# Optimization experiments

Hardware: AMD Instinct MI355X
Metric: run time of the kernel (lower is better)

Reference implementation:

```python
import jax, jax.numpy as jnp
import numpy as np

N, DIN, DOUT = 8192, 64, 32
EPS_F = 1e-6


def setup_inputs() -> dict:
    key = jax.random.key(0)
    k_x, k_q, k_lam, k_f, k_b = jax.random.split(key, 5)
    x = jax.random.normal(k_x, (N, DIN), dtype=jnp.float32)
    # Q_S stands in for the eigenvector matrix of the normalized adjacency;
    # scale by 1/sqrt(N) so columns have ~unit norm like an orthonormal basis.
    Q_S = jax.random.normal(k_q, (N, N), dtype=jnp.float32) / np.float32(np.sqrt(N))
    # Eigenvalues of D^-1/2 (A+I) D^-1/2 lie in [-1, 1].
    Lambda_S = jax.random.uniform(k_lam, (N,), dtype=jnp.float32, minval=-1.0, maxval=1.0)
    # Xavier-uniform init for F (din x din): bound = sqrt(6/(din+din))
    bound_f = np.float32(np.sqrt(6.0 / (DIN + DIN)))
    F = jax.random.uniform(k_f, (DIN, DIN), dtype=jnp.float32, minval=-bound_f, maxval=bound_f)
    # nn.Linear default init for B: U(-1/sqrt(din), 1/sqrt(din))
    bound_b = np.float32(1.0 / np.sqrt(DIN))
    B_w = jax.random.uniform(k_b, (DOUT, DIN), dtype=jnp.float32, minval=-bound_b, maxval=bound_b)
    gamma = jnp.float32(0.8)
    return {"x": x, "Q_S": Q_S, "Lambda_S": Lambda_S, "F": F, "B_w": B_w, "gamma": gamma}


def reference(x, Q_S, Lambda_S, F, B_w, gamma):
    # g(F) = F^T F / (||F^T F||_F + eps): symmetric PSD with Frobenius norm <= 1
    FF = F.T @ F
    gF = FF / (jnp.linalg.norm(FF) + EPS_F)
    lam_F, Q_F = jnp.linalg.eigh(gF)                      # [d], [d, d]
    # G[i, j] = 1 / (1 - gamma * lam_F[i] * lam_S[j])      # [d, N]
    G = 1.0 / (1.0 - gamma * lam_F[:, None] * Lambda_S[None, :])
    Xt = x.T                                              # [d, N]
    # Z = Q_F (G * (Q_F^T X^T Q_S)) Q_S^T  -- spectral-domain equilibrium solve
    Z = Q_F @ (G * (Q_F.T @ Xt @ Q_S)) @ Q_S.T            # [d, N]
    return Z.T @ B_w.T                                    # [N, dout]
```

## Files before the change

kernel.cpp:

```cpp
#include <hip/hip_runtime.h>
#include <math.h>

#define NTOT 8192
#define DDIM 64
#define DOUTD 32
#define NS_B 8
#define JS_D 8
#define KDEG 16

#define WS_GF 0
#define WS_R 4096
#define WS_S 12288
#define WS_YP 20480
#define YPSL (DDIM * NTOT)
#define WS_P (WS_YP + NS_B * YPSL)
#define WS_DP (WS_P + NTOT * DOUTD)
#define DPSL (NTOT * DOUTD)

__global__ __launch_bounds__(256) void k_prep_gF(const float* __restrict__ F,
                                                 float* __restrict__ gF) {
    __shared__ __align__(16) float Fl[64][68];
    __shared__ float red[256];
    int tid = threadIdx.x;
    for (int l = tid; l < 64 * 16; l += 256) {
        int d = l >> 4, c = (l & 15) << 2;
        *(float4*)&Fl[d][c] = *(const float4*)(F + d * 64 + c);
    }
    __syncthreads();
    int pa = tid >> 4, pb = tid & 15;
    int a0 = pa * 4, b0 = pb * 4;
    float acc[4][4] = {};
#pragma unroll 8
    for (int d = 0; d < 64; ++d) {
        float4 av = *(float4*)&Fl[d][a0];
        float4 bv = *(float4*)&Fl[d][b0];
        float aa[4] = {av.x, av.y, av.z, av.w};
        float bb[4] = {bv.x, bv.y, bv.z, bv.w};
#pragma unroll
        for (int i = 0; i < 4; ++i)
#pragma unroll
            for (int j = 0; j < 4; ++j) acc[i][j] += aa[i] * bb[j];
    }
    float ss = 0.f;
#pragma unroll
    for (int i = 0; i < 4; ++i)
#pragma unroll
        for (int j = 0; j < 4; ++j) ss += acc[i][j] * acc[i][j];
    red[tid] = ss;
    __syncthreads();
    for (int off = 128; off > 0; off >>= 1) {
        if (tid < off) red[tid] += red[tid + off];
        __syncthreads();
    }
    float scale = 1.f / (sqrtf(red[0]) + 1e-6f);
#pragma unroll
    for (int i = 0; i < 4; ++i)
#pragma unroll
        for (int j = 0; j < 4; ++j)
            gF[(a0 + i) * 64 + (b0 + j)] = acc[i][j] * scale;
}

__global__ __launch_bounds__(256) void k_prep_cols(const float* __restrict__ Lam,
                                                   const float* __restrict__ gammap,
                                                   float* __restrict__ r_arr,
                                                   float* __restrict__ s_arr) {
    int j = blockIdx.x * 256 + threadIdx.x;
    if (j < NTOT) {
        float a = gammap[0] * Lam[j];
        float q = sqrtf(fmaxf(1.f - a * a, 1e-12f));
        r_arr[j] = a / (1.f + q);
        s_arr[j] = 1.f / q;
    }
}

__global__ __launch_bounds__(256) void k_gemmB(const float* __restrict__ x,
                                               const float* __restrict__ Q,
                                               float* __restrict__ Yp) {
    __shared__ __align__(16) float xs[32][68];
    __shared__ __align__(16) float qs[32][132];
    int j0 = blockIdx.x * 128;
    int ns = blockIdx.y;
    int n0base = ns * (NTOT / NS_B);
    int tid = threadIdx.x;
    int ti = tid >> 5;
    int tj = tid & 31;
    float acc[8][4] = {};
    for (int nc = 0; nc < (NTOT / NS_B) / 32; ++nc) {
        int n0 = n0base + nc * 32;
        for (int l = tid; l < 32 * 16; l += 256) {
            int nn = l >> 4, c = (l & 15) << 2;
            *(float4*)&xs[nn][c] = *(const float4*)(x + (size_t)(n0 + nn) * 64 + c);
        }
        for (int l = tid; l < 32 * 32; l += 256) {
            int nn = l >> 5, c = (l & 31) << 2;
            *(float4*)&qs[nn][c] = *(const float4*)(Q + (size_t)(n0 + nn) * NTOT + j0 + c);
        }
        __syncthreads();
#pragma unroll 2
        for (int nn = 0; nn < 32; ++nn) {
            float4 xa = *(float4*)&xs[nn][ti * 8];
            float4 xb = *(float4*)&xs[nn][ti * 8 + 4];
            float4 qv = *(float4*)&qs[nn][tj * 4];
            float xv[8] = {xa.x, xa.y, xa.z, xa.w, xb.x, xb.y, xb.z, xb.w};
            float qq[4] = {qv.x, qv.y, qv.z, qv.w};
#pragma unroll
            for (int i = 0; i < 8; ++i)
#pragma unroll
                for (int j = 0; j < 4; ++j) acc[i][j] += xv[i] * qq[j];
        }
        __syncthreads();
    }
#pragma unroll
    for (int ii = 0; ii < 8; ++ii) {
        int i = ti * 8 + ii;
        float4 v = make_float4(acc[ii][0], acc[ii][1], acc[ii][2], acc[ii][3]);
        *(float4*)&Yp[(size_t)ns * YPSL + (size_t)i * NTOT + j0 + tj * 4] = v;
    }
}

__global__ __launch_bounds__(256) void k_cheb(const float* __restrict__ Yp,
                                              const float* __restrict__ gF,
                                              const float* __restrict__ r_arr,
                                              const float* __restrict__ s_arr,
                                              const float* __restrict__ Bw,
                                              float* __restrict__ P) {
    __shared__ __align__(16) float gfl[64][68];
    __shared__ __align__(16) float tb[2][64][34];
    __shared__ __align__(16) float bwl[32][68];
    int j0 = blockIdx.x * 32;
    int tid = threadIdx.x;
    for (int l = tid; l < 64 * 16; l += 256) {
        int k = l >> 4, c = (l & 15) << 2;
        *(float4*)&gfl[k][c] = *(const float4*)(gF + k * 64 + c);
    }
    for (int l = tid; l < 32 * 16; l += 256) {
        int o = l >> 4, c = (l & 15) << 2;
        *(float4*)&bwl[o][c] = *(const float4*)(Bw + o * 64 + c);
    }
    for (int l = tid; l < 64 * 32; l += 256) {
        int k = l >> 5, c = l & 31;
        size_t base = (size_t)k * NTOT + j0 + c;
        float v = 0.f;
#pragma unroll
        for (int p = 0; p < NS_B; ++p) v += Yp[(size_t)p * YPSL + base];
        tb[0][k][c] = v;
    }
    __syncthreads();
    int ti = tid >> 4;
    int jt = tid & 15;
    int i0 = ti * 4;
    int jc0 = j0 + jt * 2;
    float r0 = r_arr[jc0], r1 = r_arr[jc0 + 1];
    float s0 = s_arr[jc0], s1 = s_arr[jc0 + 1];
    float rp0 = 1.f, rp1 = 1.f;
    float u[4][2];
#pragma unroll
    for (int ii = 0; ii < 4; ++ii) {
        u[ii][0] = s0 * tb[0][i0 + ii][jt * 2];
        u[ii][1] = s1 * tb[0][i0 + ii][jt * 2 + 1];
    }
    int cur = 0, prv = 1;
    for (int m = 1; m <= KDEG; ++m) {
        float mv[4][2] = {};
#pragma unroll 8
        for (int k = 0; k < 64; ++k) {
            float4 g = *(float4*)&gfl[k][i0];
            float2 t = *(float2*)&tb[cur][k][jt * 2];
            mv[0][0] += g.x * t.x; mv[0][1] += g.x * t.y;
            mv[1][0] += g.y * t.x; mv[1][1] += g.y * t.y;
            mv[2][0] += g.z * t.x; mv[2][1] += g.z * t.y;
            mv[3][0] += g.w * t.x; mv[3][1] += g.w * t.y;
        }
        rp0 *= r0; rp1 *= r1;
        float c0 = 2.f * s0 * rp0, c1 = 2.f * s1 * rp1;
#pragma unroll
        for (int ii = 0; ii < 4; ++ii) {
            float t0, t1;
            if (m == 1) { t0 = mv[ii][0]; t1 = mv[ii][1]; }
            else {
                t0 = 2.f * mv[ii][0] - tb[prv][i0 + ii][jt * 2];
                t1 = 2.f * mv[ii][1] - tb[prv][i0 + ii][jt * 2 + 1];
            }
            tb[prv][i0 + ii][jt * 2] = t0;
            tb[prv][i0 + ii][jt * 2 + 1] = t1;
            u[ii][0] += c0 * t0;
            u[ii][1] += c1 * t1;
        }
        int tmp = cur; cur = prv; prv = tmp;
        __syncthreads();
    }
#pragma unroll
    for (int ii = 0; ii < 4; ++ii) {
        tb[0][i0 + ii][jt * 2] = u[ii][0];
        tb[0][i0 + ii][jt * 2 + 1] = u[ii][1];
    }
    __syncthreads();
    int jc = tid >> 3;
    int o0 = (tid & 7) * 4;
    float pacc[4] = {0.f, 0.f, 0.f, 0.f};
#pragma unroll 8
    for (int i = 0; i < 64; ++i) {
        float uv = tb[0][i][jc];
#pragma unroll
        for (int o = 0; o < 4; ++o) pacc[o] += bwl[o0 + o][i] * uv;
    }
    *(float4*)&P[(size_t)(j0 + jc) * DOUTD + o0] =
        make_float4(pacc[0], pacc[1], pacc[2], pacc[3]);
}

__global__ __launch_bounds__(256) void k_gemmD(const float* __restrict__ Q,
                                               const float* __restrict__ P,
                                               float* __restrict__ Dp) {
    __shared__ float qs[128 * 65];
    __shared__ __align__(16) float ps[64][36];
    int i0b = blockIdx.x * 128;
    int js = blockIdx.y;
    int j0s = js * (NTOT / JS_D);
    int tid = threadIdx.x;
    int ti = tid & 31;
    int to = tid >> 5;
    float acc[4][4] = {};
    for (int jt = 0; jt < (NTOT / JS_D) / 64; ++jt) {
        int j0 = j0s + jt * 64;
        for (int l = tid; l < 128 * 16; l += 256) {
            int rr = l >> 4, c = (l & 15) << 2;
            float4 v = *(const float4*)(Q + (size_t)(i0b + rr) * NTOT + j0 + c);
            float* d = &qs[rr * 65 + c];
            d[0] = v.x; d[1] = v.y; d[2] = v.z; d[3] = v.w;
        }
        for (int l = tid; l < 64 * 8; l += 256) {
            int rr = l >> 3, c = (l & 7) << 2;
            *(float4*)&ps[rr][c] = *(const float4*)(P + (size_t)(j0 + rr) * DOUTD + c);
        }
        __syncthreads();
#pragma unroll 4
        for (int j = 0; j < 64; ++j) {
            float4 pv = *(float4*)&ps[j][to * 4];
            float pp[4] = {pv.x, pv.y, pv.z, pv.w};
#pragma unroll
            for (int k = 0; k < 4; ++k) {
                float q = qs[(ti + 32 * k) * 65 + j];
#pragma unroll
                for (int o = 0; o < 4; ++o) acc[k][o] += q * pp[o];
            }
        }
        __syncthreads();
    }
#pragma unroll
    for (int k = 0; k < 4; ++k) {
        float4 v = make_float4(acc[k][0], acc[k][1], acc[k][2], acc[k][3]);
        *(float4*)&Dp[(size_t)js * DPSL + (size_t)(i0b + ti + 32 * k) * DOUTD + to * 4] = v;
    }
}

__global__ __launch_bounds__(256) void k_reduce_out(const float* __restrict__ Dp,
                                                    float* __restrict__ out) {
    int idx = (blockIdx.x * 256 + threadIdx.x) * 4;
    float4 s = *(const float4*)(Dp + idx);
#pragma unroll
    for (int p = 1; p < JS_D; ++p) {
        float4 v = *(const float4*)(Dp + (size_t)p * DPSL + idx);
        s.x += v.x; s.y += v.y; s.z += v.z; s.w += v.w;
    }
    *(float4*)(out + idx) = s;
}

extern "C" void kernel_launch(void* const* d_in, const int* in_sizes, int n_in,
                              void* d_out, int out_size, void* d_ws, size_t ws_size,
                              hipStream_t stream) {
    const float* x = (const float*)d_in[0];
    const float* Q = (const float*)d_in[1];
    const float* Lam = (const float*)d_in[2];
    const float* F = (const float*)d_in[3];
    const float* Bw = (const float*)d_in[4];
    const float* gamma = (const float*)d_in[5];
    float* ws = (float*)d_ws;
    float* gF = ws + WS_GF;
    float* r_arr = ws + WS_R;
    float* s_arr = ws + WS_S;
    float* Yp = ws + WS_YP;
    float* P = ws + WS_P;
    float* Dp = ws + WS_DP;
    float* out = (float*)d_out;

    k_prep_gF<<<1, 256, 0, stream>>>(F, gF);
    k_prep_cols<<<32, 256, 0, stream>>>(Lam, gamma, r_arr, s_arr);
    k_gemmB<<<dim3(64, NS_B), 256, 0, stream>>>(x, Q, Yp);
    k_cheb<<<256, 256, 0, stream>>>(Yp, gF, r_arr, s_arr, Bw, P);
    k_gemmD<<<dim3(64, JS_D), 256, 0, stream>>>(Q, P, Dp);
    k_reduce_out<<<256, 256, 0, stream>>>(Dp, out);
}
```

Baseline: 599.9 us.

## Restructure GEMM tilings, stream Q directly, double split-K slices, shrink Chebyshev tiles

k_gemmB now has each thread read Q from global memory as float4 and accumulate a 16x4 register tile against x staged in shared memory, instead of staging Q through LDS. The split-K factor for both big GEMMs rises from 8 to 16 when the workspace is large enough. k_cheb moves to 16-column blocks, giving twice as many blocks, and uses a transposed B_w layout. k_gemmD switches to a float4-padded Q tile with a 4-wide inner product per row. Together these aim for more parallelism and less LDS traffic on the two passes over the 256 MB Q matrix, at the cost of more partial-sum traffic and higher register pressure.

```diff
diff --git a/kernel.cpp b/kernel.cpp
--- a/kernel.cpp
+++ b/kernel.cpp
@@ -4,8 +4,6 @@
 #define NTOT 8192
 #define DDIM 64
 #define DOUTD 32
-#define NS_B 8
-#define JS_D 8
 #define KDEG 16
 
 #define WS_GF 0
@@ -13,8 +11,6 @@
 #define WS_S 12288
 #define WS_YP 20480
 #define YPSL (DDIM * NTOT)
-#define WS_P (WS_YP + NS_B * YPSL)
-#define WS_DP (WS_P + NTOT * DOUTD)
 #define DPSL (NTOT * DOUTD)
 
 __global__ __launch_bounds__(256) void k_prep_gF(const float* __restrict__ F,
@@ -76,45 +72,47 @@
 __global__ __launch_bounds__(256) void k_gemmB(const float* __restrict__ x,
                                                const float* __restrict__ Q,
                                                float* __restrict__ Yp) {
-    __shared__ __align__(16) float xs[32][68];
-    __shared__ __align__(16) float qs[32][132];
-    int j0 = blockIdx.x * 128;
+    __shared__ __align__(16) float xs[64][64];
+    int tid = threadIdx.x;
+    int jl = tid & 63;
+    int ig = tid >> 6;
+    int i0 = ig * 16;
+    int j0 = blockIdx.x * 256;
+    int jj = j0 + 4 * jl;
     int ns = blockIdx.y;
-    int n0base = ns * (NTOT / NS_B);
-    int tid = threadIdx.x;
-    int ti = tid >> 5;
-    int tj = tid & 31;
-    float acc[8][4] = {};
-    for (int nc = 0; nc < (NTOT / NS_B) / 32; ++nc) {
-        int n0 = n0base + nc * 32;
-        for (int l = tid; l < 32 * 16; l += 256) {
-            int nn = l >> 4, c = (l & 15) << 2;
-            *(float4*)&xs[nn][c] = *(const float4*)(x + (size_t)(n0 + nn) * 64 + c);
-        }
-        for (int l = tid; l < 32 * 32; l += 256) {
-            int nn = l >> 5, c = (l & 31) << 2;
-            *(float4*)&qs[nn][c] = *(const float4*)(Q + (size_t)(n0 + nn) * NTOT + j0 + c);
+    int NS = gridDim.y;
+    int nrange = NTOT / NS;
+    int n0base = ns * nrange;
+    int nchunks = nrange / 64;
+    float acc[16][4] = {};
+    for (int nc = 0; nc < nchunks; ++nc) {
+        int n0 = n0base + nc * 64;
+        __syncthreads();
+        for (int l = tid; l < 64 * 16; l += 256) {
+            int row = l >> 4, c = (l & 15) << 2;
+            *(float4*)&xs[row][c] = *(const float4*)(x + (size_t)(n0 + row) * 64 + c);
         }
         __syncthreads();
 #pragma unroll 2
-        for (int nn = 0; nn < 32; ++nn) {
-            float4 xa = *(float4*)&xs[nn][ti * 8];
-            float4 xb = *(float4*)&xs[nn][ti * 8 + 4];
-            float4 qv = *(float4*)&qs[nn][tj * 4];
-            float xv[8] = {xa.x, xa.y, xa.z, xa.w, xb.x, xb.y, xb.z, xb.w};
-            float qq[4] = {qv.x, qv.y, qv.z, qv.w};
-#pragma unroll
-            for (int i = 0; i < 8; ++i)
+        for (int nn = 0; nn < 64; ++nn) {
+            float4 q = *(const float4*)(Q + (size_t)(n0 + nn) * NTOT + jj);
+            float4 x0 = *(float4*)&xs[nn][i0];
+            float4 x1 = *(float4*)&xs[nn][i0 + 4];
+            float4 x2 = *(float4*)&xs[nn][i0 + 8];
+            float4 x3 = *(float4*)&xs[nn][i0 + 12];
+            float xv[16] = {x0.x, x0.y, x0.z, x0.w, x1.x, x1.y, x1.z, x1.w,
+                            x2.x, x2.y, x2.z, x2.w, x3.x, x3.y, x3.z, x3.w};
+            float qq[4] = {q.x, q.y, q.z, q.w};
+#pragma unroll
+            for (int i = 0; i < 16; ++i)
 #pragma unroll
                 for (int j = 0; j < 4; ++j) acc[i][j] += xv[i] * qq[j];
         }
-        __syncthreads();
-    }
-#pragma unroll
-    for (int ii = 0; ii < 8; ++ii) {
-        int i = ti * 8 + ii;
+    }
+#pragma unroll
+    for (int ii = 0; ii < 16; ++ii) {
         float4 v = make_float4(acc[ii][0], acc[ii][1], acc[ii][2], acc[ii][3]);
-        *(float4*)&Yp[(size_t)ns * YPSL + (size_t)i * NTOT + j0 + tj * 4] = v;
+        *(float4*)&Yp[(size_t)ns * YPSL + (size_t)(i0 + ii) * NTOT + jj] = v;
     }
 }
 
@@ -123,11 +121,11 @@
                                               const float* __restrict__ r_arr,
                                               const float* __restrict__ s_arr,
                                               const float* __restrict__ Bw,
-                                              float* __restrict__ P) {
+                                              float* __restrict__ P, int nslices) {
     __shared__ __align__(16) float gfl[64][68];
-    __shared__ __align__(16) float tb[2][64][34];
-    __shared__ __align__(16) float bwl[32][68];
-    int j0 = blockIdx.x * 32;
+    __shared__ float tb[2][64][18];
+    __shared__ float bwT[64][33];
+    int j0 = blockIdx.x * 16;
     int tid = threadIdx.x;
     for (int l = tid; l < 64 * 16; l += 256) {
         int k = l >> 4, c = (l & 15) << 2;
@@ -135,98 +133,84 @@
     }
     for (int l = tid; l < 32 * 16; l += 256) {
         int o = l >> 4, c = (l & 15) << 2;
-        *(float4*)&bwl[o][c] = *(const float4*)(Bw + o * 64 + c);
-    }
-    for (int l = tid; l < 64 * 32; l += 256) {
-        int k = l >> 5, c = l & 31;
-        size_t base = (size_t)k * NTOT + j0 + c;
+        float4 v = *(const float4*)(Bw + o * 64 + c);
+        bwT[c + 0][o] = v.x; bwT[c + 1][o] = v.y;
+        bwT[c + 2][o] = v.z; bwT[c + 3][o] = v.w;
+    }
+    for (int l = tid; l < 64 * 16; l += 256) {
+        int row = l >> 4, col = l & 15;
+        size_t base = (size_t)row * NTOT + j0 + col;
         float v = 0.f;
-#pragma unroll
-        for (int p = 0; p < NS_B; ++p) v += Yp[(size_t)p * YPSL + base];
-        tb[0][k][c] = v;
+        for (int p = 0; p < nslices; ++p) v += Yp[(size_t)p * YPSL + base];
+        tb[0][row][col] = v;
     }
     __syncthreads();
     int ti = tid >> 4;
     int jt = tid & 15;
     int i0 = ti * 4;
-    int jc0 = j0 + jt * 2;
-    float r0 = r_arr[jc0], r1 = r_arr[jc0 + 1];
-    float s0 = s_arr[jc0], s1 = s_arr[jc0 + 1];
-    float rp0 = 1.f, rp1 = 1.f;
-    float u[4][2];
-#pragma unroll
-    for (int ii = 0; ii < 4; ++ii) {
-        u[ii][0] = s0 * tb[0][i0 + ii][jt * 2];
-        u[ii][1] = s1 * tb[0][i0 + ii][jt * 2 + 1];
-    }
+    int jc = j0 + jt;
+    float r = r_arr[jc], s = s_arr[jc];
+    float rp = 1.f;
+    float u[4];
+#pragma unroll
+    for (int ii = 0; ii < 4; ++ii) u[ii] = s * tb[0][i0 + ii][jt];
     int cur = 0, prv = 1;
     for (int m = 1; m <= KDEG; ++m) {
-        float mv[4][2] = {};
+        float mv[4] = {};
 #pragma unroll 8
         for (int k = 0; k < 64; ++k) {
             float4 g = *(float4*)&gfl[k][i0];
-            float2 t = *(float2*)&tb[cur][k][jt * 2];
-            mv[0][0] += g.x * t.x; mv[0][1] += g.x * t.y;
-            mv[1][0] += g.y * t.x; mv[1][1] += g.y * t.y;
-            mv[2][0] += g.z * t.x; mv[2][1] += g.z * t.y;
-            mv[3][0] += g.w * t.x; mv[3][1] += g.w * t.y;
-        }
-        rp0 *= r0; rp1 *= r1;
-        float c0 = 2.f * s0 * rp0, c1 = 2.f * s1 * rp1;
+            float t = tb[cur][k][jt];
+            mv[0] += g.x * t; mv[1] += g.y * t;
+            mv[2] += g.z * t; mv[3] += g.w * t;
+        }
+        rp *= r;
+        float cm = 2.f * s * rp;
 #pragma unroll
         for (int ii = 0; ii < 4; ++ii) {
-            float t0, t1;
-            if (m == 1) { t0 = mv[ii][0]; t1 = mv[ii][1]; }
-            else {
-                t0 = 2.f * mv[ii][0] - tb[prv][i0 + ii][jt * 2];
-                t1 = 2.f * mv[ii][1] - tb[prv][i0 + ii][jt * 2 + 1];
-            }
-            tb[prv][i0 + ii][jt * 2] = t0;
-            tb[prv][i0 + ii][jt * 2 + 1] = t1;
-            u[ii][0] += c0 * t0;
-            u[ii][1] += c1 * t1;
+            float tm = (m == 1) ? mv[ii] : 2.f * mv[ii] - tb[prv][i0 + ii][jt];
+            tb[prv][i0 + ii][jt] = tm;
+            u[ii] += cm * tm;
         }
         int tmp = cur; cur = prv; prv = tmp;
         __syncthreads();
     }
 #pragma unroll
-    for (int ii = 0; ii < 4; ++ii) {
-        tb[0][i0 + ii][jt * 2] = u[ii][0];
-        tb[0][i0 + ii][jt * 2 + 1] = u[ii][1];
-    }
-    __syncthreads();
-    int jc = tid >> 3;
-    int o0 = (tid & 7) * 4;
-    float pacc[4] = {0.f, 0.f, 0.f, 0.f};
+    for (int ii = 0; ii < 4; ++ii) tb[0][i0 + ii][jt] = u[ii];
+    __syncthreads();
+    int o = tid & 31;
+    int c0 = tid >> 5;
+    float p0 = 0.f, p1 = 0.f;
 #pragma unroll 8
     for (int i = 0; i < 64; ++i) {
-        float uv = tb[0][i][jc];
-#pragma unroll
-        for (int o = 0; o < 4; ++o) pacc[o] += bwl[o0 + o][i] * uv;
-    }
-    *(float4*)&P[(size_t)(j0 + jc) * DOUTD + o0] =
-        make_float4(pacc[0], pacc[1], pacc[2], pacc[3]);
+        float b = bwT[i][o];
+        p0 += b * tb[0][i][c0];
+        p1 += b * tb[0][i][c0 + 8];
+    }
+    P[(size_t)(j0 + c0) * DOUTD + o] = p0;
+    P[(size_t)(j0 + c0 + 8) * DOUTD + o] = p1;
 }
 
 __global__ __launch_bounds__(256) void k_gemmD(const float* __restrict__ Q,
                                                const float* __restrict__ P,
                                                float* __restrict__ Dp) {
-    __shared__ float qs[128 * 65];
+    __shared__ __align__(16) float qs[128][68];
     __shared__ __align__(16) float ps[64][36];
     int i0b = blockIdx.x * 128;
     int js = blockIdx.y;
-    int j0s = js * (NTOT / JS_D);
+    int JS = gridDim.y;
+    int jrange = NTOT / JS;
+    int j0s = js * jrange;
     int tid = threadIdx.x;
     int ti = tid & 31;
     int to = tid >> 5;
     float acc[4][4] = {};
-    for (int jt = 0; jt < (NTOT / JS_D) / 64; ++jt) {
+    for (int jt = 0; jt < jrange / 64; ++jt) {
         int j0 = j0s + jt * 64;
+        __syncthreads();
         for (int l = tid; l < 128 * 16; l += 256) {
             int rr = l >> 4, c = (l & 15) << 2;
-            float4 v = *(const float4*)(Q + (size_t)(i0b + rr) * NTOT + j0 + c);
-            float* d = &qs[rr * 65 + c];
-            d[0] = v.x; d[1] = v.y; d[2] = v.z; d[3] = v.w;
+            *(float4*)&qs[rr][c] = *(const float4*)(Q + (size_t)(i0b + rr) * NTOT + j0 + c);
         }
         for (int l = tid; l < 64 * 8; l += 256) {
             int rr = l >> 3, c = (l & 7) << 2;
@@ -234,31 +218,33 @@
         }
         __syncthreads();
 #pragma unroll 4
-        for (int j = 0; j < 64; ++j) {
-            float4 pv = *(float4*)&ps[j][to * 4];
-            float pp[4] = {pv.x, pv.y, pv.z, pv.w};
-#pragma unroll
-            for (int k = 0; k < 4; ++k) {
-                float q = qs[(ti + 32 * k) * 65 + j];
-#pragma unroll
-                for (int o = 0; o < 4; ++o) acc[k][o] += q * pp[o];
+        for (int jj = 0; jj < 64; jj += 4) {
+            float4 p0 = *(float4*)&ps[jj + 0][to * 4];
+            float4 p1 = *(float4*)&ps[jj + 1][to * 4];
+            float4 p2 = *(float4*)&ps[jj + 2][to * 4];
+            float4 p3 = *(float4*)&ps[jj + 3][to * 4];
+#pragma unroll
+            for (int rr = 0; rr < 4; ++rr) {
+                float4 q = *(float4*)&qs[ti * 4 + rr][jj];
+                acc[rr][0] += q.x * p0.x + q.y * p1.x + q.z * p2.x + q.w * p3.x;
+                acc[rr][1] += q.x * p0.y + q.y * p1.y + q.z * p2.y + q.w * p3.y;
+                acc[rr][2] += q.x * p0.z + q.y * p1.z + q.z * p2.z + q.w * p3.z;
+                acc[rr][3] += q.x * p0.w + q.y * p1.w + q.z * p2.w + q.w * p3.w;
             }
         }
-        __syncthreads();
-    }
-#pragma unroll
-    for (int k = 0; k < 4; ++k) {
-        float4 v = make_float4(acc[k][0], acc[k][1], acc[k][2], acc[k][3]);
-        *(float4*)&Dp[(size_t)js * DPSL + (size_t)(i0b + ti + 32 * k) * DOUTD + to * 4] = v;
+    }
+#pragma unroll
+    for (int rr = 0; rr < 4; ++rr) {
+        float4 v = make_float4(acc[rr][0], acc[rr][1], acc[rr][2], acc[rr][3]);
+        *(float4*)&Dp[(size_t)js * DPSL + (size_t)(i0b + ti * 4 + rr) * DOUTD + to * 4] = v;
     }
 }
 
 __global__ __launch_bounds__(256) void k_reduce_out(const float* __restrict__ Dp,
-                                                    float* __restrict__ out) {
+                                                    float* __restrict__ out, int js) {
     int idx = (blockIdx.x * 256 + threadIdx.x) * 4;
     float4 s = *(const float4*)(Dp + idx);
-#pragma unroll
-    for (int p = 1; p < JS_D; ++p) {
+    for (int p = 1; p < js; ++p) {
         float4 v = *(const float4*)(Dp + (size_t)p * DPSL + idx);
         s.x += v.x; s.y += v.y; s.z += v.z; s.w += v.w;
     }
@@ -274,19 +260,24 @@
     const float* F = (const float*)d_in[3];
     const float* Bw = (const float*)d_in[4];
     const float* gamma = (const float*)d_in[5];
+
+    int NS = 16, JS = 16;
+    size_t need16 = (size_t)(WS_YP + 16 * YPSL + NTOT * DOUTD + 16 * DPSL) * 4;
+    if (ws_size < need16) { NS = 8; JS = 8; }
+
     float* ws = (float*)d_ws;
     float* gF = ws + WS_GF;
     float* r_arr = ws + WS_R;
     float* s_arr = ws + WS_S;
     float* Yp = ws + WS_YP;
-    float* P = ws + WS_P;
-    float* Dp = ws + WS_DP;
+    float* P = Yp + (size_t)NS * YPSL;
+    float* Dp = P + (size_t)NTOT * DOUTD;
     float* out = (float*)d_out;
 
     k_prep_gF<<<1, 256, 0, stream>>>(F, gF);
     k_prep_cols<<<32, 256, 0, stream>>>(Lam, gamma, r_arr, s_arr);
-    k_gemmB<<<dim3(64, NS_B), 256, 0, stream>>>(x, Q, Yp);
-    k_cheb<<<256, 256, 0, stream>>>(Yp, gF, r_arr, s_arr, Bw, P);
-    k_gemmD<<<dim3(64, JS_D), 256, 0, stream>>>(Q, P, Dp);
-    k_reduce_out<<<256, 256, 0, stream>>>(Dp, out);
-}
+    k_gemmB<<<dim3(NTOT / 256, NS), 256, 0, stream>>>(x, Q, Yp);
+    k_cheb<<<NTOT / 16, 256, 0, stream>>>(Yp, gF, r_arr, s_arr, Bw, P, NS);
+    k_gemmD<<<dim3(NTOT / 128, JS), 256, 0, stream>>>(Q, P, Dp);
+    k_reduce_out<<<NTOT * DOUTD / 4 / 256, 256, 0, stream>>>(Dp, out, JS);
+}
```

Result: slower. 696.4 us (+16.1%).
